# Optimization experiments

Hardware: AMD Instinct MI355X
Metric: run time of the kernel (lower is better)

The kernel has to match this reference:

```python
import jax, jax.numpy as jnp
import numpy as np

SEQ, B, IN, H = 512, 256, 300, 256

def setup_inputs() -> dict:
    key = jax.random.key(0)
    ks = jax.random.split(key, 14)
    s = lambda *sh: 1.0 / np.sqrt(sh[0])
    inp = {
        'secuencia': jax.random.normal(ks[0], (SEQ, B, IN), jnp.float32),
        # RNN cell 1 (forward direction)
        'W1x': jax.random.normal(ks[1], (IN, H), jnp.float32) * s(IN),
        'W1h': jax.random.normal(ks[2], (H, H), jnp.float32) * s(H),
        'b1':  jax.random.normal(ks[3], (H,), jnp.float32) * 0.01,
        # RNN cell 2 (backward direction)
        'W2x': jax.random.normal(ks[4], (IN, H), jnp.float32) * s(IN),
        'W2h': jax.random.normal(ks[5], (H, H), jnp.float32) * s(H),
        'b2':  jax.random.normal(ks[6], (H,), jnp.float32) * 0.01,
        # MLP head (weights stored [in, out])
        'fc1_w': jax.random.normal(ks[7], (2 * H, 2 * H), jnp.float32) * s(2 * H),
        'fc1_b': jnp.zeros((2 * H,), jnp.float32),
        'fc2_w': jax.random.normal(ks[8], (2 * H, H), jnp.float32) * s(2 * H),
        'fc2_b': jnp.zeros((H,), jnp.float32),
        'fs_w':  jax.random.normal(ks[9], (H, 1), jnp.float32) * s(H),
        'fs_b':  jnp.zeros((1,), jnp.float32),
    }
    return inp

def _rnn_scan(seq, Wx, Wh, b):
    # seq: [S, B, IN] -> final hidden [B, H]; Elman cell h' = tanh(x Wx + h Wh + b)
    h0 = jnp.zeros((seq.shape[1], Wh.shape[0]), seq.dtype)
    def step(h, x):
        return jnp.tanh(x @ Wx + h @ Wh + b), None
    h_final, _ = jax.lax.scan(step, h0, seq)
    return h_final

def reference(secuencia, W1x, W1h, b1, W2x, W2h, b2,
              fc1_w, fc1_b, fc2_w, fc2_b, fs_w, fs_b):
    h1 = _rnn_scan(secuencia, W1x, W1h, b1)          # forward pass over time
    h2 = _rnn_scan(secuencia[::-1], W2x, W2h, b2)    # reversed pass over time
    h = jnp.concatenate([h1, h2], axis=1)            # [B, 2H]
    x = jax.nn.relu(h @ fc1_w + fc1_b)
    x = jax.nn.relu(x @ fc2_w + fc2_b)
    out = jnp.tanh(x @ fs_w + fs_b)                  # [B, 1]
    return out.squeeze()
```

## Files before the change

### kernel.cpp

```cpp
#include <hip/hip_runtime.h>

#define DI __device__ __forceinline__

typedef float f32x4 __attribute__((ext_vector_type(4)));
typedef float f4    __attribute__((ext_vector_type(4)));
typedef _Float16 h8 __attribute__((ext_vector_type(8)));
typedef _Float16 h4 __attribute__((ext_vector_type(4)));

#define SEQL 512
#define BATCH 256
#define INF 300
#define HID 256
#define N2 512
#define KP 320


DI float ftanh(float x) {
    float e = __builtin_amdgcn_exp2f(x * 2.8853900817779268f);
    return fmaf(-2.0f, __builtin_amdgcn_rcpf(e + 1.0f), 1.0f);
}

__global__ void prep_kernel(const float* __restrict__ W1x, const float* __restrict__ W2x,
                            const float* __restrict__ b1, const float* __restrict__ b2,
                            _Float16* __restrict__ WTs, float* __restrict__ bcat)
{
    int idx = blockIdx.x * 256 + threadIdx.x;
    if (idx < N2 * KP) {
        int j = idx / KP, z = idx - j * KP;
        int k = z ^ ((j & 7) << 3);
        float v = 0.f;
        if (k < INF) v = (j < HID) ? W1x[k * HID + j] : W2x[k * HID + (j - HID)];
        WTs[j * KP + z] = (_Float16)v;
    }
    if (idx < N2) bcat[idx] = (idx < HID) ? b1[idx] : b2[idx - HID];
}

__global__ __launch_bounds__(512, 2) void gemm_pre(
    const float* __restrict__ x, const _Float16* __restrict__ WTs,
    const float* __restrict__ bcat, _Float16* __restrict__ pre3)
{
    __shared__ _Float16 AbD[2][128 * 64];
    __shared__ _Float16 BbD[2][256 * 64];
    const int tid = threadIdx.x;
    const int w = tid >> 6, l = tid & 63;
    const int lj = l & 15, lg = l >> 4;
    const int bid = blockIdx.x;
    const int xcd = bid & 7;
    const int idx0 = bid >> 3;
    const int jn = idx0 & 1;
    const int bm = xcd * 128 + (idx0 >> 1);
    const size_t m0 = (size_t)bm * 128;
    const int j0b = jn * 256;
    const int wj = (w >> 1) * 64, wm2 = (w & 1) * 64;

    f32x4 acc[4][4];
#pragma unroll
    for (int a = 0; a < 4; ++a)
#pragma unroll
        for (int b = 0; b < 4; ++b) acc[a][b] = f32x4{0.f, 0.f, 0.f, 0.f};

    char* Acur = (char*)AbD[0];
    char* Anxt = (char*)AbD[1];
    char* Bcur = (char*)BbD[0];
    char* Bnxt = (char*)BbD[1];

#define STAGE_W(K0, BDST)                                                             \
    do {                                                                              \
        _Pragma("unroll")                                                             \
        for (int q = 0; q < 4; ++q) {                                                 \
            int idx = q * 512 + tid;                                                  \
            int jr = idx >> 3, sl = idx & 7;                                          \
            const _Float16* src = WTs + (size_t)(j0b + jr) * KP + (K0) + sl * 8;      \
            _Float16* dst = (_Float16*)(BDST) + (size_t)(q * 512 + w * 64) * 8;       \
            __builtin_amdgcn_global_load_lds(                                         \
                (const __attribute__((address_space(1))) void*)src,                   \
                (__attribute__((address_space(3))) void*)dst, 16, 0, 0);              \
        }                                                                             \
    } while (0)

#define LOAD_X(K0, XR)                                                                \
    do {                                                                              \
        _Pragma("unroll")                                                             \
        for (int c = 0; c < 4; ++c) {                                                 \
            int f = c * 512 + tid;                                                    \
            int mr = f >> 4, k4 = f & 15;                                             \
            if ((K0) + k4 * 4 + 3 < INF)                                              \
                XR[c] = *(const f4*)(x + (m0 + mr) * INF + (K0) + k4 * 4);            \
            else                                                                      \
                XR[c] = f4{0.f, 0.f, 0.f, 0.f};                                       \
        }                                                                             \
    } while (0)

#define WRITE_X(XR, ADST)                                                             \
    do {                                                                              \
        _Pragma("unroll")                                                             \
        for (int c = 0; c < 4; ++c) {                                                 \
            int f = c * 512 + tid;                                                    \
            int mr = f >> 4, k4 = f & 15;                                             \
            unsigned bo = (unsigned)mr * 128 + (((unsigned)k4 * 8) ^ ((mr & 7) << 4)); \
            *(h4*)((ADST) + bo) = h4{(_Float16)XR[c][0], (_Float16)XR[c][1],          \
                                     (_Float16)XR[c][2], (_Float16)XR[c][3]};         \
        }                                                                             \
    } while (0)

#define GBARRIER()                                                                    \
    do {                                                                              \
        __builtin_amdgcn_sched_barrier(0);                                            \
        asm volatile("s_waitcnt vmcnt(0) lgkmcnt(0)" ::: "memory");                   \
        __builtin_amdgcn_s_barrier();                                                 \
        __builtin_amdgcn_sched_barrier(0);                                            \
    } while (0)

    {
        f4 xr[4];
        LOAD_X(0, xr);
        STAGE_W(0, Bcur);
        asm volatile("s_waitcnt vmcnt(4)" ::: "memory");
        WRITE_X(xr, Acur);
        GBARRIER();
    }

    for (int s = 0; s < 5; ++s) {
        f4 xr[4];
        if (s < 4) {
            const int k0n = (s + 1) * 64;
            LOAD_X(k0n, xr);
            STAGE_W(k0n, Bnxt);
        }
#pragma unroll
        for (int kk = 0; kk < 2; ++kk) {
            h8 aw[4], bx[4];
#pragma unroll
            for (int jt = 0; jt < 4; ++jt) {
                int jr = wj + jt * 16 + lj;
                unsigned bo = (unsigned)jr * 128 + (((unsigned)(kk * 64 + lg * 16)) ^ ((jr & 7) << 4));
                aw[jt] = *(const h8*)(Bcur + bo);
            }
#pragma unroll
            for (int mt = 0; mt < 4; ++mt) {
                int mr = wm2 + mt * 16 + lj;
                unsigned bo = (unsigned)mr * 128 + (((unsigned)(kk * 64 + lg * 16)) ^ ((mr & 7) << 4));
                bx[mt] = *(const h8*)(Acur + bo);
            }
#pragma unroll
            for (int jt = 0; jt < 4; ++jt)
#pragma unroll
                for (int mt = 0; mt < 4; ++mt)
                    acc[jt][mt] = __builtin_amdgcn_mfma_f32_16x16x32_f16(aw[jt], bx[mt], acc[jt][mt], 0, 0, 0);
        }
        if (s < 4) {
            asm volatile("s_waitcnt vmcnt(4)" ::: "memory");
            WRITE_X(xr, Anxt);
        }
        GBARRIER();
        char* t0 = Acur; Acur = Anxt; Anxt = t0;
        char* t1 = Bcur; Bcur = Bnxt; Bnxt = t1;
    }
#undef STAGE_W
#undef LOAD_X
#undef WRITE_X
#undef GBARRIER

    f4 bias4[4];
#pragma unroll
    for (int jt = 0; jt < 4; ++jt)
        bias4[jt] = *(const f4*)(bcat + j0b + wj + jt * 16 + lg * 4);
    char* prc = (char*)pre3;
#pragma unroll
    for (int jt = 0; jt < 4; ++jt) {
        int slab = (j0b + wj + jt * 16) >> 4;
#pragma unroll
        for (int mt = 0; mt < 4; ++mt) {
            int M = (int)m0 + wm2 + mt * 16;
            size_t byte = (size_t)(M >> 8) * 262144 + (size_t)slab * 8192
                        + (size_t)((M & 255) + lj) * 32 + (size_t)lg * 8;
            h4 o;
#pragma unroll
            for (int i = 0; i < 4; ++i)
                o[i] = (_Float16)(acc[jt][mt][i] + bias4[jt][i]);
            *(h4*)(prc + byte) = o;
        }
    }
}

__global__ __launch_bounds__(512, 2) void rnn_scan(
    const float* __restrict__ W1h, const float* __restrict__ W2h,
    const _Float16* __restrict__ pre3, float* __restrict__ hcat)
{
    __shared__ char hbs[16384];
    char* hbc = hbs;
    const int tid = threadIdx.x;
    const int w = tid >> 6, l = tid & 63;
    const int lj = l & 15, lg = l >> 4;
    const int dir = blockIdx.x & 1;
    const int b0 = (int)(blockIdx.x >> 1) * 16;
    const float* Wh = dir ? W2h : W1h;
    const int j0 = w * 32;
    const int dirOff = dir ? HID : 0;

    h8 afrag[2][8];
#pragma unroll
    for (int jt = 0; jt < 2; ++jt) {
        int jc = j0 + jt * 16 + lj;
#pragma unroll
        for (int kk = 0; kk < 8; ++kk) {
            h8 t;
#pragma unroll
            for (int i = 0; i < 8; ++i) t[i] = (_Float16)Wh[(kk * 32 + lg * 8 + i) * HID + jc];
            afrag[jt][kk] = t;
        }
    }

    const unsigned rb = (unsigned)l * 16;
    const unsigned wb0 = (unsigned)w * 1024 + (unsigned)(lg >> 1) * 256
                       + (unsigned)lj * 16 + (unsigned)(lg & 1) * 8;

    ((h8*)hbs)[tid] = h8{0, 0, 0, 0, 0, 0, 0, 0};
    __syncthreads();

    const long long sb = dir ? -262144LL : 262144LL;
    const char* pp = (const char*)pre3 + (long long)(dir ? (SEQL - 1) : 0) * 262144
                   + (long long)dir * 131072
                   + (long long)w * 16384 + (long long)(b0 + lj) * 32 + lg * 8;
    h4 pA[2], pB[2];
#pragma unroll
    for (int jt = 0; jt < 2; ++jt) pA[jt] = *(const h4*)(pp + jt * 8192);
    pp += sb;
#pragma unroll
    for (int jt = 0; jt < 2; ++jt) pB[jt] = *(const h4*)(pp + jt * 8192);
    pp += sb;

#define RD(KK, RB)                                                                    \
        bf[KK] = *(const h8*)(hbc + (RB) + (KK) * 1024 + rb);                         \
        __builtin_amdgcn_sched_barrier(0);

#define MM(KK, CNT)                                                                   \
        asm volatile("s_waitcnt lgkmcnt(" #CNT ")" ::: "memory");                     \
        __builtin_amdgcn_sched_barrier(0);                                            \
        acc0 = __builtin_amdgcn_mfma_f32_16x16x32_f16(afrag[0][KK], bf[KK], acc0, 0, 0, 0); \
        acc1 = __builtin_amdgcn_mfma_f32_16x16x32_f16(afrag[1][KK], bf[KK], acc1, 0, 0, 0);

#define RNN_STEP(RB, WB, P, DO_PF)                                                    \
    do {                                                                              \
        h8 bf[8];                                                                     \
        f32x4 acc0, acc1;                                                             \
        _Pragma("unroll")                                                             \
        for (int i = 0; i < 4; ++i) { acc0[i] = (float)P[0][i]; acc1[i] = (float)P[1][i]; } \
        __builtin_amdgcn_sched_barrier(0);                                            \
        RD(0, RB) RD(1, RB) RD(2, RB) RD(3, RB)                                       \
        RD(4, RB) RD(5, RB) RD(6, RB) RD(7, RB)                                       \
        if (DO_PF) {                                                                  \
            P[0] = *(const h4*)(pp);                                                  \
            P[1] = *(const h4*)(pp + 8192);                                           \
            pp += sb;                                                                 \
        }                                                                             \
        MM(0, 7) MM(1, 6) MM(2, 5) MM(3, 4)                                           \
        MM(4, 3) MM(5, 2) MM(6, 1) MM(7, 0)                                           \
        h4 o0, o1;                                                                    \
        _Pragma("unroll")                                                             \
        for (int i = 0; i < 4; ++i) o0[i] = (_Float16)ftanh(acc0[i]);                 \
        *(h4*)(hbc + (WB) + wb0) = o0;                                                \
        _Pragma("unroll")                                                             \
        for (int i = 0; i < 4; ++i) o1[i] = (_Float16)ftanh(acc1[i]);                 \
        *(h4*)(hbc + (WB) + wb0 + 512) = o1;                                          \
        __builtin_amdgcn_sched_barrier(0);                                            \
        asm volatile("s_waitcnt lgkmcnt(0)" ::: "memory");                            \
        __builtin_amdgcn_s_barrier();                                                 \
        __builtin_amdgcn_sched_barrier(0);                                            \
    } while (0)

    for (int tp = 0; tp < 255; ++tp) {
        RNN_STEP(0, 8192, pA, 1);
        RNN_STEP(8192, 0, pB, 1);
    }
    RNN_STEP(0, 8192, pA, 0);

    {
        f32x4 acc0, acc1;
#pragma unroll
        for (int i = 0; i < 4; ++i) { acc0[i] = (float)pB[0][i]; acc1[i] = (float)pB[1][i]; }
        h8 bf[8];
#pragma unroll
        for (int kk = 0; kk < 8; ++kk)
            bf[kk] = *(const h8*)(hbc + 8192 + kk * 1024 + rb);
#pragma unroll
        for (int kk = 0; kk < 8; ++kk) {
            acc0 = __builtin_amdgcn_mfma_f32_16x16x32_f16(afrag[0][kk], bf[kk], acc0, 0, 0, 0);
            acc1 = __builtin_amdgcn_mfma_f32_16x16x32_f16(afrag[1][kk], bf[kk], acc1, 0, 0, 0);
        }
        f4 v0, v1;
#pragma unroll
        for (int i = 0; i < 4; ++i) { v0[i] = ftanh(acc0[i]); v1[i] = ftanh(acc1[i]); }
        float* hc = hcat + (size_t)(b0 + lj) * N2 + dirOff + j0 + lg * 4;
        *(f4*)hc = v0;
        *(f4*)(hc + 16) = v1;
    }
#undef RNN_STEP
#undef MM
#undef RD
}

__global__ __launch_bounds__(256) void head_mlp(
    const float* __restrict__ hcat,
    const float* __restrict__ fc1w, const float* __restrict__ fc1b,
    const float* __restrict__ fc2w, const float* __restrict__ fc2b,
    const float* __restrict__ fsw, const float* __restrict__ fsb,
    float* __restrict__ out)
{
    __shared__ float hs[4 * 512];
    __shared__ float y1[4 * 512];
    __shared__ float y2[4 * 256];
    const int tid = threadIdx.x;
    const int b0 = blockIdx.x * 4;
    const int r = tid >> 6;
    const int lane = tid & 63;

#pragma unroll
    for (int c = 0; c < 2; ++c)
        ((f4*)hs)[c * 256 + tid] = ((const f4*)(hcat + (size_t)b0 * N2))[c * 256 + tid];
    __syncthreads();

    {
        const int j0 = lane * 8;
        f4 a0 = *(const f4*)(fc1b + j0);
        f4 a1 = *(const f4*)(fc1b + j0 + 4);
        for (int k = 0; k < 512; ++k) {
            float h = hs[r * 512 + k];
            f4 w0 = *(const f4*)(fc1w + (size_t)k * 512 + j0);
            f4 w1 = *(const f4*)(fc1w + (size_t)k * 512 + j0 + 4);
#pragma unroll
            for (int i = 0; i < 4; ++i) { a0[i] = fmaf(h, w0[i], a0[i]); a1[i] = fmaf(h, w1[i], a1[i]); }
        }
#pragma unroll
        for (int i = 0; i < 4; ++i) {
            y1[r * 512 + j0 + i]     = fmaxf(a0[i], 0.f);
            y1[r * 512 + j0 + 4 + i] = fmaxf(a1[i], 0.f);
        }
    }
    __syncthreads();

    {
        const int j2 = lane * 4;
        f4 a = *(const f4*)(fc2b + j2);
        for (int k = 0; k < 512; ++k) {
            float yv = y1[r * 512 + k];
            f4 w = *(const f4*)(fc2w + (size_t)k * 256 + j2);
#pragma unroll
            for (int i = 0; i < 4; ++i) a[i] = fmaf(yv, w[i], a[i]);
        }
#pragma unroll
        for (int i = 0; i < 4; ++i) y2[r * 256 + j2 + i] = fmaxf(a[i], 0.f);
    }
    __syncthreads();

    {
        float p = 0.f;
#pragma unroll
        for (int u = 0; u < 4; ++u)
            p = fmaf(y2[r * 256 + lane + u * 64], fsw[lane + u * 64], p);
#pragma unroll
        for (int off = 32; off > 0; off >>= 1) p += __shfl_down(p, off);
        if (lane == 0) out[b0 + r] = ftanh(p + fsb[0]);
    }
}

extern "C" void kernel_launch(void* const* d_in, const int* in_sizes, int n_in,
                              void* d_out, int out_size, void* d_ws, size_t ws_size,
                              hipStream_t stream)
{
    const float* x    = (const float*)d_in[0];
    const float* W1x  = (const float*)d_in[1];
    const float* W1h  = (const float*)d_in[2];
    const float* b1   = (const float*)d_in[3];
    const float* W2x  = (const float*)d_in[4];
    const float* W2h  = (const float*)d_in[5];
    const float* b2   = (const float*)d_in[6];
    const float* fc1w = (const float*)d_in[7];
    const float* fc1b = (const float*)d_in[8];
    const float* fc2w = (const float*)d_in[9];
    const float* fc2b = (const float*)d_in[10];
    const float* fsw  = (const float*)d_in[11];
    const float* fsb  = (const float*)d_in[12];

    char* ws = (char*)d_ws;
    size_t off = 0;
    _Float16* WTs  = (_Float16*)(ws + off); off += (size_t)N2 * KP * sizeof(_Float16);
    float* bcat    = (float*)(ws + off);    off += (size_t)N2 * sizeof(float);
    float* hcat    = (float*)(ws + off);    off += (size_t)BATCH * N2 * sizeof(float);
    _Float16* pre3 = (_Float16*)(ws + off); off += (size_t)SEQL * BATCH * N2 * sizeof(_Float16);
    if (off > ws_size) return;

    prep_kernel<<<(N2 * KP + 255) / 256, 256, 0, stream>>>(W1x, W2x, b1, b2, WTs, bcat);
    gemm_pre<<<2048, 512, 0, stream>>>(x, WTs, bcat, pre3);
    rnn_scan<<<(BATCH / 16) * 2, 512, 0, stream>>>(W1h, W2h, pre3, hcat);
    head_mlp<<<64, 256, 0, stream>>>(hcat, fc1w, fc1b, fc2w, fc2b, fsw, fsb, (float*)d_out);
}
```

Baseline: 470.9 us.

## Replace input-projection GEMM with persistent kernel keeping weight slice in LDS

```diff
diff --git a/kernel.cpp b/kernel.cpp
--- a/kernel.cpp
+++ b/kernel.cpp
@@ -33,6 +33,148 @@
         WTs[j * KP + z] = (_Float16)v;
     }
     if (idx < N2) bcat[idx] = (idx < HID) ? b1[idx] : b2[idx - HID];
+}
+
+__global__ __launch_bounds__(512, 1) void gemm_persist(
+    const float* __restrict__ x, const _Float16* __restrict__ WTs,
+    const float* __restrict__ bcat, _Float16* __restrict__ pre3)
+{
+    extern __shared__ char smem[];
+    char* Wp = smem;
+    char* Ax0 = smem + 81920;
+    char* Ax1 = smem + 81920 + 16384;
+    const int tid = threadIdx.x;
+    const int w = tid >> 6, l = tid & 63;
+    const int lj = l & 15, lg = l >> 4;
+    const int bid = blockIdx.x;
+    const int xcd = bid & 7;
+    const int idx = bid >> 3;
+    const int stripe = xcd * 8 + (idx & 7);
+    const int jq = idx >> 3;
+    const int j0b = jq * 128;
+    const int wm2 = (w & 1) * 64, wj = (w >> 1) * 32;
+
+#pragma unroll
+    for (int q = 0; q < 10; ++q) {
+        const _Float16* src = WTs + (size_t)j0b * KP + q * 4096 + (w * 64 + l) * 8;
+        _Float16* dst = (_Float16*)(Wp + q * 8192 + w * 1024);
+        __builtin_amdgcn_global_load_lds(
+            (const __attribute__((address_space(1))) void*)src,
+            (__attribute__((address_space(3))) void*)dst, 16, 0, 0);
+    }
+    asm volatile("s_waitcnt vmcnt(0)" ::: "memory");
+    __builtin_amdgcn_s_barrier();
+
+    f4 bias4[2];
+#pragma unroll
+    for (int jt = 0; jt < 2; ++jt)
+        bias4[jt] = *(const f4*)(bcat + j0b + wj + jt * 16 + lg * 4);
+
+#define LOAD_X(M0, K0, XR)                                                            \
+    do {                                                                              \
+        _Pragma("unroll")                                                             \
+        for (int c = 0; c < 4; ++c) {                                                 \
+            int f = c * 512 + tid;                                                    \
+            int mr = f >> 4, k4 = f & 15;                                             \
+            if ((K0) + k4 * 4 + 3 < INF)                                              \
+                XR[c] = *(const f4*)(x + ((M0) + mr) * INF + (K0) + k4 * 4);          \
+            else                                                                      \
+                XR[c] = f4{0.f, 0.f, 0.f, 0.f};                                       \
+        }                                                                             \
+    } while (0)
+
+#define WRITE_X(XR, ADST)                                                             \
+    do {                                                                              \
+        _Pragma("unroll")                                                             \
+        for (int c = 0; c < 4; ++c) {                                                 \
+            int f = c * 512 + tid;                                                    \
+            int mr = f >> 4, k4 = f & 15;                                             \
+            unsigned bo = (unsigned)mr * 128 + (((unsigned)k4 * 8) ^ ((mr & 7) << 4)); \
+            *(h4*)((ADST) + bo) = h4{(_Float16)XR[c][0], (_Float16)XR[c][1],          \
+                                     (_Float16)XR[c][2], (_Float16)XR[c][3]};         \
+        }                                                                             \
+    } while (0)
+
+#define GBARRIER()                                                                    \
+    do {                                                                              \
+        __builtin_amdgcn_sched_barrier(0);                                            \
+        asm volatile("s_waitcnt vmcnt(0) lgkmcnt(0)" ::: "memory");                   \
+        __builtin_amdgcn_s_barrier();                                                 \
+        __builtin_amdgcn_sched_barrier(0);                                            \
+    } while (0)
+
+    char* prc = (char*)pre3;
+
+    for (int mi = 0; mi < 16; ++mi) {
+        const int bm = stripe * 16 + mi;
+        const size_t m0 = (size_t)bm * 128;
+
+        f32x4 acc[2][4];
+#pragma unroll
+        for (int a = 0; a < 2; ++a)
+#pragma unroll
+            for (int b = 0; b < 4; ++b) acc[a][b] = f32x4{0.f, 0.f, 0.f, 0.f};
+
+        char* Acur = Ax0;
+        char* Anxt = Ax1;
+        {
+            f4 xr[4];
+            LOAD_X(m0, 0, xr);
+            asm volatile("s_waitcnt vmcnt(0)" ::: "memory");
+            WRITE_X(xr, Acur);
+            GBARRIER();
+        }
+        for (int s = 0; s < 5; ++s) {
+            f4 xr[4];
+            if (s < 4) LOAD_X(m0, (s + 1) * 64, xr);
+#pragma unroll
+            for (int kk = 0; kk < 2; ++kk) {
+                h8 aw[2], bx[4];
+#pragma unroll
+                for (int jt = 0; jt < 2; ++jt) {
+                    int jr = wj + jt * 16 + lj;
+                    unsigned bo = (unsigned)jr * 640 + (unsigned)s * 128
+                                + (((unsigned)(kk * 64 + lg * 16)) ^ ((jr & 7) << 4));
+                    aw[jt] = *(const h8*)(Wp + bo);
+                }
+#pragma unroll
+                for (int mt = 0; mt < 4; ++mt) {
+                    int mr = wm2 + mt * 16 + lj;
+                    unsigned bo = (unsigned)mr * 128 + (((unsigned)(kk * 64 + lg * 16)) ^ ((mr & 7) << 4));
+                    bx[mt] = *(const h8*)(Acur + bo);
+                }
+#pragma unroll
+                for (int jt = 0; jt < 2; ++jt)
+#pragma unroll
+                    for (int mt = 0; mt < 4; ++mt)
+                        acc[jt][mt] = __builtin_amdgcn_mfma_f32_16x16x32_f16(aw[jt], bx[mt], acc[jt][mt], 0, 0, 0);
+            }
+            if (s < 4) {
+                asm volatile("s_waitcnt vmcnt(0)" ::: "memory");
+                WRITE_X(xr, Anxt);
+            }
+            GBARRIER();
+            char* t0 = Acur; Acur = Anxt; Anxt = t0;
+        }
+#pragma unroll
+        for (int jt = 0; jt < 2; ++jt) {
+            int slab = (j0b + wj + jt * 16) >> 4;
+#pragma unroll
+            for (int mt = 0; mt < 4; ++mt) {
+                int M = (int)m0 + wm2 + mt * 16;
+                size_t byte = (size_t)(M >> 8) * 262144 + (size_t)slab * 8192
+                            + (size_t)((M & 255) + lj) * 32 + (size_t)lg * 8;
+                h4 o;
+#pragma unroll
+                for (int i = 0; i < 4; ++i)
+                    o[i] = (_Float16)(acc[jt][mt][i] + bias4[jt][i]);
+                *(h4*)(prc + byte) = o;
+            }
+        }
+    }
+#undef LOAD_X
+#undef WRITE_X
+#undef GBARRIER
 }
 
 __global__ __launch_bounds__(512, 2) void gemm_pre(
@@ -119,7 +261,6 @@
         WRITE_X(xr, Acur);
         GBARRIER();
     }
-
     for (int s = 0; s < 5; ++s) {
         f4 xr[4];
         if (s < 4) {
@@ -391,7 +532,14 @@
     if (off > ws_size) return;
 
     prep_kernel<<<(N2 * KP + 255) / 256, 256, 0, stream>>>(W1x, W2x, b1, b2, WTs, bcat);
-    gemm_pre<<<2048, 512, 0, stream>>>(x, WTs, bcat, pre3);
+
+    static hipError_t attr_err = hipFuncSetAttribute(
+        (const void*)gemm_persist, hipFuncAttributeMaxDynamicSharedMemorySize, 114688);
+    if (attr_err == hipSuccess) {
+        gemm_persist<<<256, 512, 114688, stream>>>(x, WTs, bcat, pre3);
+    } else {
+        gemm_pre<<<2048, 512, 0, stream>>>(x, WTs, bcat, pre3);
+    }
     rnn_scan<<<(BATCH / 16) * 2, 512, 0, stream>>>(W1h, W2h, pre3, hcat);
     head_mlp<<<64, 256, 0, stream>>>(hcat, fc1w, fc1b, fc2w, fc2b, fsw, fsb, (float*)d_out);
 }
```

After: 527.9 us. +12.1%, slower.
